# Performance work log

Hardware: AMD Instinct MI355X
Metric: run time of the kernel (lower is better)

## Reference

```python
import jax, jax.numpy as jnp
import numpy as np

NEG_SLOPE = 0.2


def _leaky_relu(v):
    return jnp.where(v >= 0, v, NEG_SLOPE * v)


def setup_inputs() -> dict:
    key = jax.random.key(0)
    ks = jax.random.split(key, 12)
    N_items, F_in, Hd, Do = 16384, 128, 128, 64
    N_nodes, E = 8192, 524288
    g = lambda k, s: (jax.random.normal(k, s, dtype=jnp.float32)
                      * np.float32(1.0 / np.sqrt(s[0])))
    return {
        "x": jax.random.normal(ks[0], (N_items, F_in), dtype=jnp.float32),
        "H": jax.random.uniform(ks[1], (N_nodes, N_items), dtype=jnp.float32),
        "edge_index": jax.random.randint(ks[2], (2, E), 0, N_items, dtype=jnp.int64),
        "W_gat": g(ks[3], (F_in, Hd)),
        "a_src": g(ks[4], (Hd,)),
        "a_dst": g(ks[5], (Hd,)),
        "b_gat": jnp.zeros((Hd,), dtype=jnp.float32),
        "W_etn": g(ks[6], (Hd, Hd)),
        "b_etn": jnp.zeros((Hd,), dtype=jnp.float32),
        "W_lin": g(ks[7], (Hd, Do)),
    }


def _gat(x, edge_index, W_gat, a_src, a_dst, b_gat):
    # PyG GATConv, heads=1: linear transform, edge attention softmax at target,
    # self-loops added.
    N = x.shape[0]
    h = x @ W_gat                                   # [N, Hd]
    loop = jnp.arange(N, dtype=edge_index.dtype)
    src = jnp.concatenate([edge_index[0], loop])    # [E+N]
    dst = jnp.concatenate([edge_index[1], loop])
    alpha = _leaky_relu((h @ a_src)[src] + (h @ a_dst)[dst])  # [E+N]
    # numerically stable segment softmax over incoming edges of each target
    m = jax.ops.segment_max(alpha, dst, num_segments=N)
    e = jnp.exp(alpha - m[dst])
    denom = jax.ops.segment_sum(e, dst, num_segments=N)
    w = e / denom[dst]
    out = jax.ops.segment_sum(h[src] * w[:, None], dst, num_segments=N)
    return out + b_gat


def reference(x, H, edge_index, W_gat, a_src, a_dst, b_gat, W_etn, b_etn, W_lin):
    gat_out = _gat(x, edge_index, W_gat, a_src, a_dst, b_gat)   # [N_items, Hd]
    # Edge-to-node conv: incidence aggregation then linear
    out = (H @ gat_out) @ W_etn + b_etn                         # [N_nodes, Hd]
    out = _leaky_relu(out)
    return out @ W_lin                                          # [N_nodes, Do]
```

## Files before the change

### kernel.cpp

```cpp
#include <hip/hip_runtime.h>
#include <hip/hip_bf16.h>


#define NEG 0.2f
#define N_ITEMS 16384
#define N_NODES 8192
#define E_EDGES 524288
#define HD 128

typedef float f32x4 __attribute__((ext_vector_type(4)));
typedef short bf16x8 __attribute__((ext_vector_type(8)));

__device__ __forceinline__ float leaky(float v) { return v >= 0.0f ? v : NEG * v; }

__device__ __forceinline__ unsigned short f2bf(float f) {
  unsigned int u = __float_as_uint(f);
  u += 0x7FFFu + ((u >> 16) & 1u);
  return (unsigned short)(u >> 16);
}

__global__ __launch_bounds__(256) void k_zero(f32x4* p, int n4) {
  int i = blockIdx.x * 256 + threadIdx.x;
  int stride = gridDim.x * 256;
  f32x4 z = {0.0f, 0.0f, 0.0f, 0.0f};
  for (; i < n4; i += stride) p[i] = z;
}

__global__ __launch_bounds__(256) void k_h(const float* __restrict__ x,
                                           const float* __restrict__ Wg,
                                           float* __restrict__ h) {
  int gid = blockIdx.x * 256 + threadIdx.x;
  int row = gid >> 5;
  int c4 = (gid & 31) * 4;
  const float* xr = x + (size_t)row * 128;
  f32x4 acc = {0.0f, 0.0f, 0.0f, 0.0f};
  for (int k = 0; k < 128; k++) {
    float xv = xr[k];
    f32x4 w = *(const f32x4*)&Wg[k * 128 + c4];
    acc += xv * w;
  }
  *(f32x4*)&h[(size_t)row * 128 + c4] = acc;
}

__global__ __launch_bounds__(256) void k_hsd(const float* __restrict__ h,
                                             const float* __restrict__ a_src,
                                             const float* __restrict__ a_dst,
                                             float* __restrict__ hs, float* __restrict__ hd) {
  int r = blockIdx.x * 4 + (threadIdx.x >> 6);
  int lane = threadIdx.x & 63;
  float v0 = h[(size_t)r * 128 + lane];
  float v1 = h[(size_t)r * 128 + 64 + lane];
  float s = v0 * a_src[lane] + v1 * a_src[64 + lane];
  float d = v0 * a_dst[lane] + v1 * a_dst[64 + lane];
  for (int off = 32; off; off >>= 1) { s += __shfl_down(s, off); d += __shfl_down(d, off); }
  if (lane == 0) { hs[r] = s; hd[r] = d; }
}

__global__ __launch_bounds__(256) void k_hist(const int* __restrict__ ei,
                                              int* __restrict__ cnt) {
  int e = blockIdx.x * 256 + threadIdx.x;
  if (e < E_EDGES) atomicAdd(&cnt[ei[E_EDGES + e]], 1);
}

__global__ __launch_bounds__(256) void k_scan(const int* __restrict__ cnt,
                                              int* __restrict__ off,
                                              int* __restrict__ cur) {
  __shared__ int part[256];
  int t = threadIdx.x;
  int base = t * 64;
  int sum = 0;
  for (int i = 0; i < 64; i++) sum += cnt[base + i];
  part[t] = sum;
  __syncthreads();
  for (int o = 1; o < 256; o <<= 1) {
    int v = (t >= o) ? part[t - o] : 0;
    __syncthreads();
    part[t] += v;
    __syncthreads();
  }
  int run = (t > 0) ? part[t - 1] : 0;
  for (int i = 0; i < 64; i++) {
    off[base + i] = run;
    cur[base + i] = run;
    run += cnt[base + i];
  }
  if (t == 255) off[16384] = run;
}

__global__ __launch_bounds__(256) void k_reorder(const int* __restrict__ ei,
                                                 int* __restrict__ cur,
                                                 int* __restrict__ es) {
  int e = blockIdx.x * 256 + threadIdx.x;
  if (e >= E_EDGES) return;
  int d = ei[E_EDGES + e];
  int pos = atomicAdd(&cur[d], 1);
  es[pos] = ei[e];
}

__global__ __launch_bounds__(256) void k_agg(const int* __restrict__ es,
                                             const int* __restrict__ off,
                                             const float* __restrict__ hs,
                                             const float* __restrict__ hd,
                                             const float* __restrict__ h,
                                             const float* __restrict__ b_gat,
                                             float* __restrict__ gat) {
  int d = blockIdx.x * 4 + (threadIdx.x >> 6);
  int lane = threadIdx.x & 63;
  int beg = off[d], end = off[d + 1];
  float hdd = hd[d];
  float m = leaky(hs[d] + hdd);
  float l = 1.0f;
  float acc0 = h[(size_t)d * 128 + lane];
  float acc1 = h[(size_t)d * 128 + 64 + lane];

  for (int j0 = beg; j0 < end; j0 += 64) {
    int n = end - j0; if (n > 64) n = 64;
    int s = (lane < n) ? es[j0 + lane] : 0;
    float a = (lane < n) ? leaky(hs[s] + hdd) : -3.0e38f;
    float cm = a;
    for (int o = 32; o; o >>= 1) cm = fmaxf(cm, __shfl_down(cm, o));
    cm = __shfl(cm, 0);
    float nm = fmaxf(m, cm);
    float scale = __expf(m - nm);
    acc0 *= scale; acc1 *= scale; l *= scale;
    m = nm;
    float w = (lane < n) ? __expf(a - nm) : 0.0f;
    float wsum = w;
    for (int o = 32; o; o >>= 1) wsum += __shfl_down(wsum, o);
    l += __shfl(wsum, 0);
    for (int j = 0; j < n; j++) {
      float wj = __shfl(w, j);
      int sj = __shfl(s, j);
      const float* hr = h + (size_t)sj * 128;
      acc0 = fmaf(wj, hr[lane], acc0);
      acc1 = fmaf(wj, hr[64 + lane], acc1);
    }
  }
  float inv = 1.0f / l;
  gat[(size_t)d * 128 + lane]      = acc0 * inv + b_gat[lane];
  gat[(size_t)d * 128 + 64 + lane] = acc1 * inv + b_gat[64 + lane];
}

__global__ __launch_bounds__(256) void k_cvt(const float* __restrict__ gat,
                                             unsigned short* __restrict__ Gt) {
  __shared__ unsigned short T[128][65];
  int r0 = blockIdx.x * 64;
  int t = threadIdx.x;
#pragma unroll
  for (int i = 0; i < 32; i++) {
    int flat = i * 256 + t;
    int r = flat >> 7, c = flat & 127;
    T[c][r] = f2bf(gat[(size_t)(r0 + r) * 128 + c]);
  }
  __syncthreads();
#pragma unroll
  for (int i = 0; i < 32; i++) {
    int flat = i * 256 + t;
    int c = flat >> 6, r = flat & 63;
    Gt[(size_t)c * 16384 + r0 + r] = T[c][r];
  }
}

#define GB_LDA 72
#define GB_LDB 72

__device__ __forceinline__ f32x4 mfma16(bf16x8 a, bf16x8 b, f32x4 c) {
  return __builtin_amdgcn_mfma_f32_16x16x32_bf16(a, b, c, 0, 0, 0);
}

__global__ __launch_bounds__(256, 4) void k_gemm_big(const float* __restrict__ Hm,
                                                     const unsigned short* __restrict__ Gt,
                                                     float* __restrict__ C1) {
  __shared__ __align__(16) unsigned short As[32 * GB_LDA];
  __shared__ __align__(16) unsigned short Bs[128 * GB_LDB];

  const int g = blockIdx.x & 7;
  const int ksplit = g & 3;
  const int mt = ((blockIdx.x >> 3) << 1) | (g >> 2);
  const int m0 = mt * 32;
  const int kbeg = ksplit * 4096;

  const int t = threadIdx.x;
  const int lane = t & 63;
  const int wave = t >> 6;
  const int wm = wave & 1;
  const int wn = wave >> 1;

  f32x4 acc0 = {0,0,0,0}, acc1 = {0,0,0,0}, acc2 = {0,0,0,0}, acc3 = {0,0,0,0};

  const int ar = t >> 3;
  const int ac = (t & 7) * 8;
  const float* Ap = Hm + (size_t)(m0 + ar) * 16384 + ac + kbeg;
  unsigned short* AsW = &As[ar * GB_LDA + ac];

  const int bc = t >> 1;
  const int bsg = (t & 1) * 32;
  const unsigned short* Bp = Gt + (size_t)bc * 16384 + bsg + kbeg;
  unsigned short* BsW = &Bs[bc * GB_LDB + bsg];

  const unsigned short* AsR = &As[(wm * 16 + (lane & 15)) * GB_LDA + (lane >> 4) * 8];
  const unsigned short* BsR = &Bs[(wn * 64 + (lane & 15)) * GB_LDB + (lane >> 4) * 8];

  for (int k0 = 0; k0 < 4096; k0 += 64) {
    f32x4 a0 = *(const f32x4*)(Ap + k0);
    f32x4 a1 = *(const f32x4*)(Ap + k0 + 4);
    bf16x8 b0 = *(const bf16x8*)(Bp + k0);
    bf16x8 b1 = *(const bf16x8*)(Bp + k0 + 8);
    bf16x8 b2 = *(const bf16x8*)(Bp + k0 + 16);
    bf16x8 b3 = *(const bf16x8*)(Bp + k0 + 24);
    bf16x8 av;
    av[0] = (short)f2bf(a0[0]); av[1] = (short)f2bf(a0[1]);
    av[2] = (short)f2bf(a0[2]); av[3] = (short)f2bf(a0[3]);
    av[4] = (short)f2bf(a1[0]); av[5] = (short)f2bf(a1[1]);
    av[6] = (short)f2bf(a1[2]); av[7] = (short)f2bf(a1[3]);

    __syncthreads();
    *(bf16x8*)AsW = av;
    *(bf16x8*)(BsW)      = b0;
    *(bf16x8*)(BsW + 8)  = b1;
    *(bf16x8*)(BsW + 16) = b2;
    *(bf16x8*)(BsW + 24) = b3;
    __syncthreads();

#pragma unroll
    for (int kk = 0; kk < 2; kk++) {
      bf16x8 af = *(const bf16x8*)(AsR + kk * 32);
      acc0 = mfma16(af, *(const bf16x8*)(BsR + kk * 32), acc0);
      acc1 = mfma16(af, *(const bf16x8*)(BsR + 16 * GB_LDB + kk * 32), acc1);
      acc2 = mfma16(af, *(const bf16x8*)(BsR + 32 * GB_LDB + kk * 32), acc2);
      acc3 = mfma16(af, *(const bf16x8*)(BsR + 48 * GB_LDB + kk * 32), acc3);
    }
  }

  const int erow = m0 + wm * 16 + ((lane >> 4) << 2);
  const int ecol = wn * 64 + (lane & 15);
  f32x4 accs[4] = {acc0, acc1, acc2, acc3};
#pragma unroll
  for (int nt = 0; nt < 4; nt++)
#pragma unroll
    for (int r = 0; r < 4; r++)
      atomicAdd(&C1[(size_t)(erow + r) * 128 + ecol + nt * 16], accs[nt][r]);
}

__global__ __launch_bounds__(256) void k_final(const float* __restrict__ C1,
                                               const float* __restrict__ We,
                                               const float* __restrict__ be,
                                               const float* __restrict__ Wl,
                                               float* __restrict__ out) {
  __shared__ float t1[32][132];
  const int t = threadIdx.x;
  const int r0 = blockIdx.x * 32;
  const int r = t >> 3;
  const int cg = (t & 7) * 16;
  const float* cr = C1 + (size_t)(r0 + r) * 128;
  f32x4 acc[4] = {{0,0,0,0},{0,0,0,0},{0,0,0,0},{0,0,0,0}};
  for (int k = 0; k < 128; k++) {
    float cv = cr[k];
    const f32x4* wrow = (const f32x4*)&We[k * 128 + cg];
    acc[0] += cv * wrow[0];
    acc[1] += cv * wrow[1];
    acc[2] += cv * wrow[2];
    acc[3] += cv * wrow[3];
  }
#pragma unroll
  for (int j = 0; j < 16; j++) {
    float v = acc[j >> 2][j & 3] + be[cg + j];
    t1[r][cg + j] = leaky(v);
  }
  __syncthreads();
  const int c8 = (t & 7) * 8;
  f32x4 acc2[2] = {{0,0,0,0},{0,0,0,0}};
  for (int k = 0; k < 128; k++) {
    float tv = t1[r][k];
    const f32x4* wl = (const f32x4*)&Wl[k * 64 + c8];
    acc2[0] += tv * wl[0];
    acc2[1] += tv * wl[1];
  }
#pragma unroll
  for (int j = 0; j < 8; j++)
    out[(size_t)(r0 + r) * 64 + c8 + j] = acc2[j >> 2][j & 3];
}

extern "C" void kernel_launch(void* const* d_in, const int* in_sizes, int n_in,
                              void* d_out, int out_size, void* d_ws, size_t ws_size,
                              hipStream_t stream) {
  const float* x      = (const float*)d_in[0];
  const float* Hm     = (const float*)d_in[1];
  const int*   ei     = (const int*)d_in[2];
  const float* Wg     = (const float*)d_in[3];
  const float* a_src  = (const float*)d_in[4];
  const float* a_dst  = (const float*)d_in[5];
  const float* b_gat  = (const float*)d_in[6];
  const float* We     = (const float*)d_in[7];
  const float* be     = (const float*)d_in[8];
  const float* Wl     = (const float*)d_in[9];
  float* out = (float*)d_out;

  char* ws = (char*)d_ws;
  float*          h     = (float*)(ws);
  float*          gat   = (float*)(ws + 8388608);
  float*          hs    = (float*)(ws + 16777216);
  float*          hd    = (float*)(ws + 16842752);
  int*            cnt   = (int*)  (ws + 16908288);
  int*            off   = (int*)  (ws + 16973824);
  int*            cur   = (int*)  (ws + 17104896);
  int*            es    = (int*)  (ws + 17170432);
  unsigned short* Gt    = (unsigned short*)ws;
  float*          C1    = (float*)(ws + 8388608);

  k_zero<<<64, 256, 0, stream>>>((f32x4*)cnt, 4096);
  k_h<<<2048, 256, 0, stream>>>(x, Wg, h);
  k_hsd<<<4096, 256, 0, stream>>>(h, a_src, a_dst, hs, hd);
  k_hist<<<E_EDGES / 256, 256, 0, stream>>>(ei, cnt);
  k_scan<<<1, 256, 0, stream>>>(cnt, off, cur);
  k_reorder<<<E_EDGES / 256, 256, 0, stream>>>(ei, cur, es);
  k_agg<<<4096, 256, 0, stream>>>(es, off, hs, hd, h, b_gat, gat);
  k_cvt<<<256, 256, 0, stream>>>(gat, Gt);
  k_zero<<<1024, 256, 0, stream>>>((f32x4*)C1, 262144);
  k_gemm_big<<<1024, 256, 0, stream>>>(Hm, Gt, C1);
  k_final<<<256, 256, 0, stream>>>(C1, We, be, Wl, out);
}
```

Measured before the change: 957.3 us.

## Fuse attention-score projection into h GEMM and tune scan, agg, final kernels

Merges the k_hsd attention-coefficient kernel into k_h, which now stages W_gat in shared memory and computes h plus the src/dst scores with a lane shuffle reduction. This drops one launch and a re-read of h. The single-block scan moves to 1024 threads with vectorized loads, the aggregation loop is unrolled by two to overlap gathers, and k_final is retiled with W_lin staged in shared memory. The 64KB shared buffer in k_h limits occupancy. The dominant big GEMM is unchanged, so the overall effect is bounded.

```diff
diff --git a/kernel.cpp b/kernel.cpp
--- a/kernel.cpp
+++ b/kernel.cpp
@@ -10,6 +10,7 @@
 
 typedef float f32x4 __attribute__((ext_vector_type(4)));
 typedef short bf16x8 __attribute__((ext_vector_type(8)));
+typedef int i32x4 __attribute__((ext_vector_type(4)));
 
 __device__ __forceinline__ float leaky(float v) { return v >= 0.0f ? v : NEG * v; }
 
@@ -28,32 +29,49 @@
 
 __global__ __launch_bounds__(256) void k_h(const float* __restrict__ x,
                                            const float* __restrict__ Wg,
-                                           float* __restrict__ h) {
-  int gid = blockIdx.x * 256 + threadIdx.x;
-  int row = gid >> 5;
-  int c4 = (gid & 31) * 4;
-  const float* xr = x + (size_t)row * 128;
-  f32x4 acc = {0.0f, 0.0f, 0.0f, 0.0f};
+                                           const float* __restrict__ a_src,
+                                           const float* __restrict__ a_dst,
+                                           float* __restrict__ h,
+                                           float* __restrict__ hs,
+                                           float* __restrict__ hd) {
+  __shared__ float Wgs[128 * 128];
+  const int t = threadIdx.x;
+#pragma unroll
+  for (int i = 0; i < 16; i++) {
+    int idx = (i * 256 + t) * 4;
+    *(f32x4*)&Wgs[idx] = *(const f32x4*)&Wg[idx];
+  }
+  __syncthreads();
+
+  const int r = blockIdx.x * 32 + (t >> 3);
+  const int cg = (t & 7) * 16;
+  const float* xr = x + (size_t)r * 128;
+  f32x4 acc[4] = {{0,0,0,0},{0,0,0,0},{0,0,0,0},{0,0,0,0}};
   for (int k = 0; k < 128; k++) {
     float xv = xr[k];
-    f32x4 w = *(const f32x4*)&Wg[k * 128 + c4];
-    acc += xv * w;
-  }
-  *(f32x4*)&h[(size_t)row * 128 + c4] = acc;
-}
-
-__global__ __launch_bounds__(256) void k_hsd(const float* __restrict__ h,
-                                             const float* __restrict__ a_src,
-                                             const float* __restrict__ a_dst,
-                                             float* __restrict__ hs, float* __restrict__ hd) {
-  int r = blockIdx.x * 4 + (threadIdx.x >> 6);
-  int lane = threadIdx.x & 63;
-  float v0 = h[(size_t)r * 128 + lane];
-  float v1 = h[(size_t)r * 128 + 64 + lane];
-  float s = v0 * a_src[lane] + v1 * a_src[64 + lane];
-  float d = v0 * a_dst[lane] + v1 * a_dst[64 + lane];
-  for (int off = 32; off; off >>= 1) { s += __shfl_down(s, off); d += __shfl_down(d, off); }
-  if (lane == 0) { hs[r] = s; hd[r] = d; }
+    const f32x4* wr = (const f32x4*)&Wgs[k * 128 + cg];
+    acc[0] += xv * wr[0];
+    acc[1] += xv * wr[1];
+    acc[2] += xv * wr[2];
+    acc[3] += xv * wr[3];
+  }
+  float* hrow = h + (size_t)r * 128 + cg;
+  *(f32x4*)(hrow)      = acc[0];
+  *(f32x4*)(hrow + 4)  = acc[1];
+  *(f32x4*)(hrow + 8)  = acc[2];
+  *(f32x4*)(hrow + 12) = acc[3];
+
+  float s = 0.0f, d = 0.0f;
+#pragma unroll
+  for (int j = 0; j < 16; j++) {
+    float hv = acc[j >> 2][j & 3];
+    s += hv * a_src[cg + j];
+    d += hv * a_dst[cg + j];
+  }
+  s += __shfl_xor(s, 1); d += __shfl_xor(d, 1);
+  s += __shfl_xor(s, 2); d += __shfl_xor(d, 2);
+  s += __shfl_xor(s, 4); d += __shfl_xor(d, 4);
+  if ((t & 7) == 0) { hs[r] = s; hd[r] = d; }
 }
 
 __global__ __launch_bounds__(256) void k_hist(const int* __restrict__ ei,
@@ -62,29 +80,37 @@
   if (e < E_EDGES) atomicAdd(&cnt[ei[E_EDGES + e]], 1);
 }
 
-__global__ __launch_bounds__(256) void k_scan(const int* __restrict__ cnt,
-                                              int* __restrict__ off,
-                                              int* __restrict__ cur) {
-  __shared__ int part[256];
-  int t = threadIdx.x;
-  int base = t * 64;
+__global__ __launch_bounds__(1024) void k_scan(const int* __restrict__ cnt,
+                                               int* __restrict__ off,
+                                               int* __restrict__ cur) {
+  __shared__ int part[1024];
+  const int t = threadIdx.x;
+  const int base = t * 16;
+  i32x4 c[4];
+#pragma unroll
+  for (int i = 0; i < 4; i++) c[i] = *(const i32x4*)&cnt[base + i * 4];
   int sum = 0;
-  for (int i = 0; i < 64; i++) sum += cnt[base + i];
+#pragma unroll
+  for (int i = 0; i < 4; i++) sum += c[i][0] + c[i][1] + c[i][2] + c[i][3];
   part[t] = sum;
   __syncthreads();
-  for (int o = 1; o < 256; o <<= 1) {
+  for (int o = 1; o < 1024; o <<= 1) {
     int v = (t >= o) ? part[t - o] : 0;
     __syncthreads();
     part[t] += v;
     __syncthreads();
   }
   int run = (t > 0) ? part[t - 1] : 0;
-  for (int i = 0; i < 64; i++) {
-    off[base + i] = run;
-    cur[base + i] = run;
-    run += cnt[base + i];
-  }
-  if (t == 255) off[16384] = run;
+#pragma unroll
+  for (int i = 0; i < 4; i++)
+#pragma unroll
+    for (int j = 0; j < 4; j++) {
+      int idx = base + i * 4 + j;
+      off[idx] = run;
+      cur[idx] = run;
+      run += c[i][j];
+    }
+  if (t == 1023) off[16384] = run;
 }
 
 __global__ __launch_bounds__(256) void k_reorder(const int* __restrict__ ei,
@@ -128,12 +154,18 @@
     float wsum = w;
     for (int o = 32; o; o >>= 1) wsum += __shfl_down(wsum, o);
     l += __shfl(wsum, 0);
-    for (int j = 0; j < n; j++) {
-      float wj = __shfl(w, j);
-      int sj = __shfl(s, j);
-      const float* hr = h + (size_t)sj * 128;
-      acc0 = fmaf(wj, hr[lane], acc0);
-      acc1 = fmaf(wj, hr[64 + lane], acc1);
+    int nn = (n + 1) & ~1;
+    for (int j = 0; j < nn; j += 2) {
+      float w0 = __shfl(w, j);     int s0 = __shfl(s, j);
+      float w1 = __shfl(w, j + 1); int s1 = __shfl(s, j + 1);
+      const float* h0 = h + (size_t)s0 * 128;
+      const float* h1 = h + (size_t)s1 * 128;
+      float a00 = h0[lane], a01 = h0[64 + lane];
+      float a10 = h1[lane], a11 = h1[64 + lane];
+      acc0 = fmaf(w0, a00, acc0);
+      acc1 = fmaf(w0, a01, acc1);
+      acc0 = fmaf(w1, a10, acc0);
+      acc1 = fmaf(w1, a11, acc1);
     }
   }
   float inv = 1.0f / l;
@@ -247,38 +279,38 @@
                                                const float* __restrict__ be,
                                                const float* __restrict__ Wl,
                                                float* __restrict__ out) {
-  __shared__ float t1[32][132];
+  __shared__ float t1[16][132];
+  __shared__ float Wls[8192];
   const int t = threadIdx.x;
-  const int r0 = blockIdx.x * 32;
-  const int r = t >> 3;
-  const int cg = (t & 7) * 16;
+#pragma unroll
+  for (int i = 0; i < 8; i++) {
+    int idx = (i * 256 + t) * 4;
+    *(f32x4*)&Wls[idx] = *(const f32x4*)&Wl[idx];
+  }
+  const int r0 = blockIdx.x * 16;
+  const int r = t >> 4;
+  const int cg = (t & 15) * 8;
   const float* cr = C1 + (size_t)(r0 + r) * 128;
-  f32x4 acc[4] = {{0,0,0,0},{0,0,0,0},{0,0,0,0},{0,0,0,0}};
+  f32x4 acc[2] = {{0,0,0,0},{0,0,0,0}};
   for (int k = 0; k < 128; k++) {
     float cv = cr[k];
     const f32x4* wrow = (const f32x4*)&We[k * 128 + cg];
     acc[0] += cv * wrow[0];
     acc[1] += cv * wrow[1];
-    acc[2] += cv * wrow[2];
-    acc[3] += cv * wrow[3];
-  }
-#pragma unroll
-  for (int j = 0; j < 16; j++) {
+  }
+#pragma unroll
+  for (int j = 0; j < 8; j++) {
     float v = acc[j >> 2][j & 3] + be[cg + j];
     t1[r][cg + j] = leaky(v);
   }
   __syncthreads();
-  const int c8 = (t & 7) * 8;
-  f32x4 acc2[2] = {{0,0,0,0},{0,0,0,0}};
+  const int c4 = (t & 15) * 4;
+  f32x4 acc2 = {0,0,0,0};
   for (int k = 0; k < 128; k++) {
     float tv = t1[r][k];
-    const f32x4* wl = (const f32x4*)&Wl[k * 64 + c8];
-    acc2[0] += tv * wl[0];
-    acc2[1] += tv * wl[1];
-  }
-#pragma unroll
-  for (int j = 0; j < 8; j++)
-    out[(size_t)(r0 + r) * 64 + c8 + j] = acc2[j >> 2][j & 3];
+    acc2 += tv * *(const f32x4*)&Wls[k * 64 + c4];
+  }
+  *(f32x4*)&out[(size_t)(r0 + r) * 64 + c4] = acc2;
 }
 
 extern "C" void kernel_launch(void* const* d_in, const int* in_sizes, int n_in,
@@ -309,14 +341,13 @@
   float*          C1    = (float*)(ws + 8388608);
 
   k_zero<<<64, 256, 0, stream>>>((f32x4*)cnt, 4096);
-  k_h<<<2048, 256, 0, stream>>>(x, Wg, h);
-  k_hsd<<<4096, 256, 0, stream>>>(h, a_src, a_dst, hs, hd);
+  k_h<<<512, 256, 0, stream>>>(x, Wg, a_src, a_dst, h, hs, hd);
   k_hist<<<E_EDGES / 256, 256, 0, stream>>>(ei, cnt);
-  k_scan<<<1, 256, 0, stream>>>(cnt, off, cur);
+  k_scan<<<1, 1024, 0, stream>>>(cnt, off, cur);
   k_reorder<<<E_EDGES / 256, 256, 0, stream>>>(ei, cur, es);
   k_agg<<<4096, 256, 0, stream>>>(es, off, hs, hd, h, b_gat, gat);
   k_cvt<<<256, 256, 0, stream>>>(gat, Gt);
   k_zero<<<1024, 256, 0, stream>>>((f32x4*)C1, 262144);
   k_gemm_big<<<1024, 256, 0, stream>>>(Hm, Gt, C1);
-  k_final<<<256, 256, 0, stream>>>(C1, We, be, Wl, out);
-}
+  k_final<<<512, 256, 0, stream>>>(C1, We, be, Wl, out);
+}
```

After: 889.7 us. 7.1% less time.
